# Performance work log

Hardware: AMD Instinct MI355X
Metric: run time of the kernel (lower is better)

Reference implementation:

```python
import jax, jax.numpy as jnp
import numpy as np
import math

B, S, D = 4, 2048, 1024
WINDOW = 10  # window_size; attends to |i-j| <= WINDOW//2


def setup_inputs() -> dict:
    key = jax.random.key(0)
    ks = jax.random.split(key, 9)
    sc = 1.0 / math.sqrt(D)
    return {
        "x": jax.random.normal(ks[0], (B, S, D), dtype=jnp.float32),
        "Wq": jax.random.normal(ks[1], (D, D), dtype=jnp.float32) * sc,
        "bq": jnp.zeros((D,), dtype=jnp.float32),
        "Wk": jax.random.normal(ks[2], (D, D), dtype=jnp.float32) * sc,
        "bk": jnp.zeros((D,), dtype=jnp.float32),
        "Wv": jax.random.normal(ks[3], (D, D), dtype=jnp.float32) * sc,
        "bv": jnp.zeros((D,), dtype=jnp.float32),
        "Wo": jax.random.normal(ks[4], (D, D), dtype=jnp.float32) * sc,
        "bo": jnp.zeros((D,), dtype=jnp.float32),
    }


def _local_mask(seq_len: int, window_size: int) -> jnp.ndarray:
    # row i attends to columns [i - w//2, i + w//2] inclusive -> |i - j| <= w//2
    i = jnp.arange(seq_len)[:, None]
    j = jnp.arange(seq_len)[None, :]
    return jnp.abs(i - j) <= (window_size // 2)  # [S, S] bool


def reference(x, Wq, bq, Wk, bk, Wv, bv, Wo, bo):
    # nn.Linear: y = x @ W.T + b
    Q = x @ Wq.T + bq  # [B, S, D]
    K = x @ Wk.T + bk
    V = x @ Wv.T + bv
    scores = jnp.einsum("bqd,bkd->bqk", Q, K) / jnp.float32(math.sqrt(D))
    mask = _local_mask(x.shape[1], WINDOW)
    scores = jnp.where(mask[None, :, :], scores, jnp.float32(-1e9))
    attn = jax.nn.softmax(scores, axis=-1)  # [B, S, S]
    context = jnp.einsum("bqk,bkd->bqd", attn, V)
    output = context @ Wo.T + bo
    return output, attn
```

## Files before the change

### kernel.cpp

```cpp
#include <hip/hip_runtime.h>
#include <hip/hip_bf16.h>
#include <cstdint>
#include <cstddef>


typedef __attribute__((ext_vector_type(8))) short bf16x8;
typedef __attribute__((ext_vector_type(4))) float f32x4;
typedef __attribute__((ext_vector_type(8))) unsigned short ushortx8;

#define GPTR(x) ((const __attribute__((address_space(1))) void*)(x))
#define LPTR(x) ((__attribute__((address_space(3))) void*)(x))

__device__ __forceinline__ unsigned short f2bf(float f) {
    __hip_bfloat16 h = __float2bfloat16(f);
    unsigned short u;
    __builtin_memcpy(&u, &h, 2);
    return u;
}
__device__ __forceinline__ float bf2f(unsigned short u) {
    unsigned int x = ((unsigned int)u) << 16;
    float f;
    __builtin_memcpy(&f, &x, 4);
    return f;
}

__global__ void prep1(const float* __restrict__ x,  const float* __restrict__ Wq,
                      const float* __restrict__ Wk, const float* __restrict__ Wv,
                      const float* __restrict__ Wo, const float* __restrict__ bv,
                      unsigned short* __restrict__ xh,
                      unsigned short* __restrict__ Woh,
                      unsigned short* __restrict__ Wqt,
                      unsigned short* __restrict__ Wkt,
                      unsigned short* __restrict__ Wvt,
                      float* __restrict__ bvo) {
    __shared__ float tl[64][65];
    const int bid = blockIdx.x;
    if (bid < 9216) {
        const int idx = bid * 256 + threadIdx.x;
        const float* src;
        unsigned short* dst;
        int off;
        if (idx < 2097152) { src = x;  dst = xh;  off = idx; }
        else               { src = Wo; dst = Woh; off = idx - 2097152; }
        f32x4 v = reinterpret_cast<const f32x4*>(src)[off];
        ushort4 o;
        o.x = f2bf(v[0]); o.y = f2bf(v[1]); o.z = f2bf(v[2]); o.w = f2bf(v[3]);
        reinterpret_cast<ushort4*>(dst)[off] = o;
    } else if (bid < 9984) {
        const int u   = bid - 9216;
        const int z   = u >> 8;
        const int rem = u & 255;
        const int by  = rem >> 4;
        const int bx  = rem & 15;
        const float* in = (z == 0) ? Wq : (z == 1) ? Wk : Wv;
        unsigned short* out = (z == 0) ? Wqt : (z == 1) ? Wkt : Wvt;
        const int t  = threadIdx.x;
        const int c  = t & 63;
        const int r4 = t >> 6;
#pragma unroll
        for (int i = 0; i < 16; ++i) {
            const int r = r4 * 16 + i;
            tl[r][c] = in[(size_t)(by * 64 + r) * 1024 + bx * 64 + c];
        }
        __syncthreads();
#pragma unroll
        for (int i = 0; i < 16; ++i) {
            const int r = r4 * 16 + i;
            out[(size_t)(bx * 64 + r) * 1024 + by * 64 + c] = f2bf(tl[c][r]);
        }
    } else {
        const int row  = (bid - 9984) * 4 + (threadIdx.x >> 6);
        const int lane = threadIdx.x & 63;
        float s = 0.f;
#pragma unroll
        for (int k = lane; k < 1024; k += 64)
            s += Wo[(size_t)row * 1024 + k] * bv[k];
#pragma unroll
        for (int off = 32; off >= 1; off >>= 1) s += __shfl_xor(s, off, 64);
        if (lane == 0) bvo[row] = s;
    }
}

__device__ __forceinline__ void gemm_core(const unsigned short* __restrict__ A,
                                          const unsigned short* __restrict__ Bw,
                                          int Kstride, int nk, int tm, int tn,
                                          unsigned short* As, unsigned short* Bs,
                                          f32x4 (&acc)[4][4]) {
    const int tid  = threadIdx.x;
    const int lane = tid & 63;
    const int w    = tid >> 6;
    const int wr   = w >> 1;
    const int wc   = w & 1;

    const int lrow8 = lane >> 3;
    const int lcolb = (lane & 7) << 4;

    const char* Abase = (const char*)(A + (size_t)tm * 128 * (size_t)Kstride);
    const char* Bbase = (const char*)(Bw + (size_t)tn * 128 * (size_t)Kstride);
    const size_t rstride = (size_t)Kstride * 2;

    for (int t = 0; t < nk; ++t) {
        const size_t k0b = ((size_t)t << 6) * 2;
#pragma unroll
        for (int ii = 0; ii < 4; ++ii) {
            const int c    = (w << 2) + ii;
            const int row  = (c << 3) + lrow8;
            const int csrc = lcolb ^ ((row & 7) << 4);
            __builtin_amdgcn_global_load_lds(
                GPTR(Abase + (size_t)row * rstride + k0b + (size_t)csrc),
                LPTR((char*)As + (c << 10)), 16, 0, 0);
            __builtin_amdgcn_global_load_lds(
                GPTR(Bbase + (size_t)row * rstride + k0b + (size_t)csrc),
                LPTR((char*)Bs + (c << 10)), 16, 0, 0);
        }
        __syncthreads();

#pragma unroll
        for (int kk = 0; kk < 2; ++kk) {
            bf16x8 af[4], bfr[4];
            const int cb = (kk << 6) + ((lane >> 4) << 4);
#pragma unroll
            for (int m = 0; m < 4; ++m) {
                const int row = (wr << 6) + (m << 4) + (lane & 15);
                af[m] = *reinterpret_cast<const bf16x8*>(
                    (const char*)As + row * 128 + (cb ^ ((row & 7) << 4)));
            }
#pragma unroll
            for (int n = 0; n < 4; ++n) {
                const int row = (wc << 6) + (n << 4) + (lane & 15);
                bfr[n] = *reinterpret_cast<const bf16x8*>(
                    (const char*)Bs + row * 128 + (cb ^ ((row & 7) << 4)));
            }
#pragma unroll
            for (int m = 0; m < 4; ++m)
#pragma unroll
                for (int n = 0; n < 4; ++n)
                    acc[m][n] = __builtin_amdgcn_mfma_f32_16x16x32_bf16(
                        af[m], bfr[n], acc[m][n], 0, 0, 0);
        }
        __syncthreads();
    }
}

__launch_bounds__(256, 3)
__global__ void splitk(const unsigned short* __restrict__ Wqt,
                       const unsigned short* __restrict__ Wkt,
                       const unsigned short* __restrict__ Woh,
                       const unsigned short* __restrict__ Wvt,
                       float* __restrict__ part) {
    __shared__ unsigned short As[128 * 64];
    __shared__ unsigned short Bs[128 * 64];
    f32x4 acc[4][4];
#pragma unroll
    for (int m = 0; m < 4; ++m)
#pragma unroll
        for (int n = 0; n < 4; ++n) acc[m][n] = (f32x4){0.f, 0.f, 0.f, 0.f};

    const int bid = blockIdx.x;
    const int mat = bid >> 8;
    const int loc = bid & 255;
    const int ks  = loc >> 6;
    const int t64 = loc & 63;
    const int tm  = t64 >> 3;
    const int tn  = t64 & 7;

    const unsigned short* A = mat ? Woh : Wqt;
    const unsigned short* B = mat ? Wvt : Wkt;
    gemm_core(A + ks * 256, B + ks * 256, 1024, 4, tm, tn, As, Bs, acc);

    float* dst = part + ((size_t)(mat * 4 + ks) << 20);
    const int lane = threadIdx.x & 63;
    const int w    = threadIdx.x >> 6;
    const int wr   = w >> 1, wc = w & 1;
    const int col0 = (tn << 7) + (wc << 6) + (lane & 15);
    const int row0 = (tm << 7) + (wr << 6) + ((lane >> 4) << 2);
#pragma unroll
    for (int n = 0; n < 4; ++n) {
        const int col = col0 + (n << 4);
#pragma unroll
        for (int m = 0; m < 4; ++m) {
            const int row = row0 + (m << 4);
#pragma unroll
            for (int r = 0; r < 4; ++r)
                dst[(size_t)(row + r) * 1024 + col] = acc[m][n][r];
        }
    }
}

__launch_bounds__(256, 4)
__global__ void redgemv(const float* __restrict__ part,
                        unsigned short* __restrict__ W2,
                        const unsigned short* __restrict__ Wqt,
                        const unsigned short* __restrict__ Wkt,
                        const float* __restrict__ bq, const float* __restrict__ bk,
                        float* __restrict__ w1, float* __restrict__ w2,
                        float* __restrict__ cbuf) {
    const int bid = blockIdx.x;
    if (bid < 2048) {
        const int u = bid * 256 + threadIdx.x;
        const int mat = u >> 18;
        const int off = u & 262143;
        const f32x4* p = reinterpret_cast<const f32x4*>(part);
        f32x4 s = p[((size_t)(mat * 4 + 0) << 18) + off];
        s += p[((size_t)(mat * 4 + 1) << 18) + off];
        s += p[((size_t)(mat * 4 + 2) << 18) + off];
        s += p[((size_t)(mat * 4 + 3) << 18) + off];
        ushort4 o;
        o.x = f2bf(s[0]); o.y = f2bf(s[1]); o.z = f2bf(s[2]); o.w = f2bf(s[3]);
        reinterpret_cast<ushort4*>(W2)[u] = o;
        return;
    }
    if (bid == 2304) {
        __shared__ float red[256];
        float pc = 0.f;
        for (int n = threadIdx.x; n < 1024; n += 256) pc += bq[n] * bk[n];
        red[threadIdx.x] = pc;
        __syncthreads();
        for (int s = 128; s > 0; s >>= 1) {
            if (threadIdx.x < s) red[threadIdx.x] += red[threadIdx.x + s];
            __syncthreads();
        }
        if (threadIdx.x == 0) cbuf[0] = red[0];
        return;
    }
    const int w    = threadIdx.x >> 6;
    const int lane = threadIdx.x & 63;
    const int d    = (bid - 2048) * 4 + w;
    const int n0   = lane << 4;
    const unsigned short* krow = Wkt + (size_t)d * 1024 + n0;
    const unsigned short* qrow = Wqt + (size_t)d * 1024 + n0;
    ushortx8 ka = *reinterpret_cast<const ushortx8*>(krow);
    ushortx8 kb = *reinterpret_cast<const ushortx8*>(krow + 8);
    ushortx8 qa = *reinterpret_cast<const ushortx8*>(qrow);
    ushortx8 qb = *reinterpret_cast<const ushortx8*>(qrow + 8);
    float a1 = 0.f, a2 = 0.f;
#pragma unroll
    for (int t = 0; t < 8; ++t) {
        a1 += bq[n0 + t] * bf2f(ka[t]) + bq[n0 + 8 + t] * bf2f(kb[t]);
        a2 += bk[n0 + t] * bf2f(qa[t]) + bk[n0 + 8 + t] * bf2f(qb[t]);
    }
#pragma unroll
    for (int off = 32; off >= 1; off >>= 1) {
        a1 += __shfl_xor(a1, off, 64);
        a2 += __shfl_xor(a2, off, 64);
    }
    if (lane == 0) { w1[d] = a1; w2[d] = a2; }
}

__launch_bounds__(256, 4)
__global__ void yv_r12(const unsigned short* __restrict__ A,
                       const unsigned short* __restrict__ Bw,
                       const float* __restrict__ bvo,
                       unsigned short* __restrict__ C,
                       const unsigned short* __restrict__ xh,
                       const float* __restrict__ w1, const float* __restrict__ w2,
                       const float* __restrict__ cbuf,
                       float* __restrict__ r1, float* __restrict__ r2) {
    __shared__ unsigned short As[128 * 64];
    __shared__ unsigned short Bs[128 * 64];
    const int bid = blockIdx.x;
    if (bid >= 1024) {
        const int w    = threadIdx.x >> 6;
        const int lane = threadIdx.x & 63;
        const int g    = (bid - 1024) * 4 + w;
        const unsigned short* row = xh + (size_t)g * 1024 + (lane << 4);
        ushortx8 xa = *reinterpret_cast<const ushortx8*>(row);
        ushortx8 xb = *reinterpret_cast<const ushortx8*>(row + 8);
        float a1 = 0.f, a2 = 0.f;
#pragma unroll
        for (int t = 0; t < 8; ++t) {
            const float xv = bf2f(xa[t]);
            const float xw = bf2f(xb[t]);
            a1 += xv * w1[(lane << 4) + t] + xw * w1[(lane << 4) + 8 + t];
            a2 += xv * w2[(lane << 4) + t] + xw * w2[(lane << 4) + 8 + t];
        }
#pragma unroll
        for (int off = 32; off >= 1; off >>= 1) {
            a1 += __shfl_xor(a1, off, 64);
            a2 += __shfl_xor(a2, off, 64);
        }
        if (lane == 0) { r1[g] = a1 + cbuf[0]; r2[g] = a2; }
        return;
    }

    f32x4 acc[4][4];
#pragma unroll
    for (int m = 0; m < 4; ++m)
#pragma unroll
        for (int n = 0; n < 4; ++n) acc[m][n] = (f32x4){0.f, 0.f, 0.f, 0.f};

    const int sid = (bid & 7) * 128 + (bid >> 3);
    const int tm  = sid >> 4;
    const int tn  = sid & 15;

    gemm_core(A, Bw, 1024, 16, tm, tn, As, Bs, acc);

    const int lane = threadIdx.x & 63;
    const int w    = threadIdx.x >> 6;
    const int wr   = w >> 1, wc = w & 1;
    const int seg  = tn >> 3;
    const int col0 = (tn << 7) + (wc << 6) + (lane & 15);
    const int row0 = (tm << 7) + (wr << 6) + ((lane >> 4) << 2);
#pragma unroll
    for (int n = 0; n < 4; ++n) {
        const int col = col0 + (n << 4);
        const float bb = seg ? bvo[col & 1023] : 0.f;
#pragma unroll
        for (int m = 0; m < 4; ++m) {
            const int row = row0 + (m << 4);
#pragma unroll
            for (int r = 0; r < 4; ++r)
                C[(size_t)(row + r) * 2048 + col] = f2bf(acc[m][n][r] + bb);
        }
    }
}

__launch_bounds__(256, 4)
__global__ void attn_band_kernel(const unsigned short* __restrict__ xh,
                                 const unsigned short* __restrict__ yVp,
                                 const float* __restrict__ r1,
                                 const float* __restrict__ r2,
                                 const float* __restrict__ bo,
                                 float* __restrict__ attn,
                                 float* __restrict__ outp) {
    __shared__ float psm[4][16];
    const int bid  = blockIdx.x;
    const int rb   = (bid & 7) * 256 + (bid >> 3);
    const int w    = threadIdx.x >> 6;
    const int lane = threadIdx.x & 63;
    const int g    = (rb << 2) + w;
    const int b    = g >> 11;
    const int i    = g & 2047;

    const unsigned short* qrow = xh + (size_t)g * 1024;
    float qf[16];
    {
        ushortx8 qa = *reinterpret_cast<const ushortx8*>(qrow + (lane << 4));
        ushortx8 qb = *reinterpret_cast<const ushortx8*>(qrow + (lane << 4) + 8);
#pragma unroll
        for (int t = 0; t < 8; ++t) { qf[t] = bf2f(qa[t]); qf[8 + t] = bf2f(qb[t]); }
    }
    const float r2g = r2[g];

    float s[11];
#pragma unroll
    for (int jj = 0; jj < 11; ++jj) {
        const int j = i - 5 + jj;
        const bool valid = ((unsigned)j < 2048u);
        const int jc = min(max(j, 0), 2047);
        const int gj = (b << 11) + jc;
        const unsigned short* krow = yVp + (size_t)gj * 2048;
        ushortx8 ka = *reinterpret_cast<const ushortx8*>(krow + (lane << 4));
        ushortx8 kb = *reinterpret_cast<const ushortx8*>(krow + (lane << 4) + 8);
        float d = 0.f;
#pragma unroll
        for (int t = 0; t < 8; ++t)
            d += qf[t] * bf2f(ka[t]) + qf[8 + t] * bf2f(kb[t]);
#pragma unroll
        for (int off = 32; off >= 1; off >>= 1) d += __shfl_xor(d, off, 64);
        s[jj] = valid ? (d + r2g + r1[gj]) * 0.03125f : -1e30f;
    }

    float mx = s[0];
#pragma unroll
    for (int jj = 1; jj < 11; ++jj) mx = fmaxf(mx, s[jj]);
    float p[11], sum = 0.f;
#pragma unroll
    for (int jj = 0; jj < 11; ++jj) { p[jj] = expf(s[jj] - mx); sum += p[jj]; }
    const float inv = 1.0f / sum;

    if (lane == 0) {
#pragma unroll
        for (int jj = 0; jj < 11; ++jj) psm[w][jj] = p[jj] * inv;
    }
    __syncthreads();

    const int lo = i - 5;
    float* arow = attn + (size_t)g * 2048;
#pragma unroll
    for (int e = 0; e < 8; ++e) {
        const int c0 = (e << 8) + (lane << 2);
        f32x4 v = (f32x4){0.f, 0.f, 0.f, 0.f};
        if (c0 + 3 >= lo && c0 <= lo + 10) {
#pragma unroll
            for (int t = 0; t < 4; ++t) {
                const int d = c0 + t - lo;
                if ((unsigned)d < 11u) v[t] = psm[w][d];
            }
        }
        *reinterpret_cast<f32x4*>(arow + c0) = v;
    }

    float cacc[16];
#pragma unroll
    for (int t = 0; t < 16; ++t) cacc[t] = 0.f;
#pragma unroll
    for (int jj = 0; jj < 11; ++jj) {
        const int j  = i - 5 + jj;
        const int jc = min(max(j, 0), 2047);
        const float pj = p[jj] * inv;
        const unsigned short* vrow = yVp + ((size_t)((b << 11) + jc)) * 2048 + 1024;
        ushortx8 va = *reinterpret_cast<const ushortx8*>(vrow + (lane << 4));
        ushortx8 vb = *reinterpret_cast<const ushortx8*>(vrow + (lane << 4) + 8);
#pragma unroll
        for (int t = 0; t < 8; ++t) {
            cacc[t]     += pj * bf2f(va[t]);
            cacc[8 + t] += pj * bf2f(vb[t]);
        }
    }
    const int c0 = lane << 4;
    float* op = outp + (size_t)g * 1024 + c0;
#pragma unroll
    for (int q = 0; q < 4; ++q) {
        f32x4 bb = *reinterpret_cast<const f32x4*>(bo + c0 + (q << 2));
        f32x4 o;
#pragma unroll
        for (int t = 0; t < 4; ++t) o[t] = cacc[(q << 2) + t] + bb[t];
        *reinterpret_cast<f32x4*>(op + (q << 2)) = o;
    }
}

extern "C" void kernel_launch(void* const* d_in, const int* in_sizes, int n_in,
                              void* d_out, int out_size, void* d_ws, size_t ws_size,
                              hipStream_t stream) {
    const float* x  = (const float*)d_in[0];
    const float* Wq = (const float*)d_in[1];
    const float* bq = (const float*)d_in[2];
    const float* Wk = (const float*)d_in[3];
    const float* bk = (const float*)d_in[4];
    const float* Wv = (const float*)d_in[5];
    const float* bv = (const float*)d_in[6];
    const float* Wo = (const float*)d_in[7];
    const float* bo = (const float*)d_in[8];

    const size_t MS = 8192, DD = 1024;

    float* out  = (float*)d_out;
    float* attn = out + MS * DD;

    char* ws = (char*)d_ws;
    unsigned short* xh   = (unsigned short*)ws; ws += MS * DD * 2;
    unsigned short* Woh  = (unsigned short*)ws; ws += DD * DD * 2;
    unsigned short* Wqt  = (unsigned short*)ws; ws += DD * DD * 2;
    unsigned short* Wkt  = (unsigned short*)ws; ws += DD * DD * 2;
    unsigned short* Wvt  = (unsigned short*)ws; ws += DD * DD * 2;
    float*          bvo  = (float*)ws;          ws += DD * 4;
    float*          w1   = (float*)ws;          ws += DD * 4;
    float*          w2   = (float*)ws;          ws += DD * 4;
    float*          cbuf = (float*)ws;          ws += 256;
    float*          r1   = (float*)ws;          ws += MS * 4;
    float*          r2   = (float*)ws;          ws += MS * 4;
    float*          part = (float*)ws;          ws += (size_t)8 * DD * DD * 4;
    unsigned short* W2   = (unsigned short*)ws; ws += 2 * DD * DD * 2;
    unsigned short* yVp  = (unsigned short*)ws; ws += MS * 2 * DD * 2;

    prep1<<<dim3(10240), dim3(256), 0, stream>>>(x, Wq, Wk, Wv, Wo, bv,
                                                 xh, Woh, Wqt, Wkt, Wvt, bvo);

    splitk<<<dim3(512), dim3(256), 0, stream>>>(Wqt, Wkt, Woh, Wvt, part);

    redgemv<<<dim3(2305), dim3(256), 0, stream>>>(part, W2, Wqt, Wkt, bq, bk,
                                                  w1, w2, cbuf);

    yv_r12<<<dim3(3072), dim3(256), 0, stream>>>(xh, W2, bvo, yVp,
                                                 xh, w1, w2, cbuf, r1, r2);

    attn_band_kernel<<<dim3(2048), dim3(256), 0, stream>>>(xh, yVp, r1, r2, bo,
                                                           attn, out);
}
```

Measured before the change: 119.1 us.

## Overlap x conversion and bias GEMVs with split-K weight GEMM blocks

```diff
diff --git a/kernel.cpp b/kernel.cpp
--- a/kernel.cpp
+++ b/kernel.cpp
@@ -24,32 +24,17 @@
     return f;
 }
 
-__global__ void prep1(const float* __restrict__ x,  const float* __restrict__ Wq,
-                      const float* __restrict__ Wk, const float* __restrict__ Wv,
-                      const float* __restrict__ Wo, const float* __restrict__ bv,
-                      unsigned short* __restrict__ xh,
-                      unsigned short* __restrict__ Woh,
+__global__ void prepW(const float* __restrict__ Wq, const float* __restrict__ Wk,
+                      const float* __restrict__ Wv, const float* __restrict__ Wo,
                       unsigned short* __restrict__ Wqt,
                       unsigned short* __restrict__ Wkt,
                       unsigned short* __restrict__ Wvt,
-                      float* __restrict__ bvo) {
+                      unsigned short* __restrict__ Woh) {
     __shared__ float tl[64][65];
     const int bid = blockIdx.x;
-    if (bid < 9216) {
-        const int idx = bid * 256 + threadIdx.x;
-        const float* src;
-        unsigned short* dst;
-        int off;
-        if (idx < 2097152) { src = x;  dst = xh;  off = idx; }
-        else               { src = Wo; dst = Woh; off = idx - 2097152; }
-        f32x4 v = reinterpret_cast<const f32x4*>(src)[off];
-        ushort4 o;
-        o.x = f2bf(v[0]); o.y = f2bf(v[1]); o.z = f2bf(v[2]); o.w = f2bf(v[3]);
-        reinterpret_cast<ushort4*>(dst)[off] = o;
-    } else if (bid < 9984) {
-        const int u   = bid - 9216;
-        const int z   = u >> 8;
-        const int rem = u & 255;
+    if (bid < 768) {
+        const int z   = bid >> 8;
+        const int rem = bid & 255;
         const int by  = rem >> 4;
         const int bx  = rem & 15;
         const float* in = (z == 0) ? Wq : (z == 1) ? Wk : Wv;
@@ -69,15 +54,11 @@
             out[(size_t)(bx * 64 + r) * 1024 + by * 64 + c] = f2bf(tl[c][r]);
         }
     } else {
-        const int row  = (bid - 9984) * 4 + (threadIdx.x >> 6);
-        const int lane = threadIdx.x & 63;
-        float s = 0.f;
-#pragma unroll
-        for (int k = lane; k < 1024; k += 64)
-            s += Wo[(size_t)row * 1024 + k] * bv[k];
-#pragma unroll
-        for (int off = 32; off >= 1; off >>= 1) s += __shfl_xor(s, off, 64);
-        if (lane == 0) bvo[row] = s;
+        const int off = (bid - 768) * 256 + threadIdx.x;
+        f32x4 v = reinterpret_cast<const f32x4*>(Wo)[off];
+        ushort4 o;
+        o.x = f2bf(v[0]); o.y = f2bf(v[1]); o.z = f2bf(v[2]); o.w = f2bf(v[3]);
+        reinterpret_cast<ushort4*>(Woh)[off] = o;
     }
 }
 
@@ -143,20 +124,81 @@
 }
 
 __launch_bounds__(256, 3)
-__global__ void splitk(const unsigned short* __restrict__ Wqt,
-                       const unsigned short* __restrict__ Wkt,
-                       const unsigned short* __restrict__ Woh,
-                       const unsigned short* __restrict__ Wvt,
-                       float* __restrict__ part) {
+__global__ void skx(const unsigned short* __restrict__ Wqt,
+                    const unsigned short* __restrict__ Wkt,
+                    const unsigned short* __restrict__ Woh,
+                    const unsigned short* __restrict__ Wvt,
+                    float* __restrict__ part,
+                    const float* __restrict__ x, unsigned short* __restrict__ xh,
+                    const float* __restrict__ Wo, const float* __restrict__ bv,
+                    float* __restrict__ bvo,
+                    const float* __restrict__ bq, const float* __restrict__ bk,
+                    float* __restrict__ w1, float* __restrict__ w2,
+                    float* __restrict__ cbuf) {
     __shared__ unsigned short As[128 * 64];
     __shared__ unsigned short Bs[128 * 64];
+    const int bid = blockIdx.x;
+    if (bid >= 512) {
+        if (bid < 8704) {
+            const int off = (bid - 512) * 256 + threadIdx.x;
+            f32x4 v = reinterpret_cast<const f32x4*>(x)[off];
+            ushort4 o;
+            o.x = f2bf(v[0]); o.y = f2bf(v[1]); o.z = f2bf(v[2]); o.w = f2bf(v[3]);
+            reinterpret_cast<ushort4*>(xh)[off] = o;
+        } else if (bid < 8960) {
+            const int row  = (bid - 8704) * 4 + (threadIdx.x >> 6);
+            const int lane = threadIdx.x & 63;
+            float s = 0.f;
+#pragma unroll
+            for (int k = lane; k < 1024; k += 64)
+                s += Wo[(size_t)row * 1024 + k] * bv[k];
+#pragma unroll
+            for (int off = 32; off >= 1; off >>= 1) s += __shfl_xor(s, off, 64);
+            if (lane == 0) bvo[row] = s;
+        } else if (bid < 9216) {
+            const int w    = threadIdx.x >> 6;
+            const int lane = threadIdx.x & 63;
+            const int d    = (bid - 8960) * 4 + w;
+            const int n0   = lane << 4;
+            const unsigned short* krow = Wkt + (size_t)d * 1024 + n0;
+            const unsigned short* qrow = Wqt + (size_t)d * 1024 + n0;
+            ushortx8 ka = *reinterpret_cast<const ushortx8*>(krow);
+            ushortx8 kb = *reinterpret_cast<const ushortx8*>(krow + 8);
+            ushortx8 qa = *reinterpret_cast<const ushortx8*>(qrow);
+            ushortx8 qb = *reinterpret_cast<const ushortx8*>(qrow + 8);
+            float a1 = 0.f, a2 = 0.f;
+#pragma unroll
+            for (int t = 0; t < 8; ++t) {
+                a1 += bq[n0 + t] * bf2f(ka[t]) + bq[n0 + 8 + t] * bf2f(kb[t]);
+                a2 += bk[n0 + t] * bf2f(qa[t]) + bk[n0 + 8 + t] * bf2f(qb[t]);
+            }
+#pragma unroll
+            for (int off = 32; off >= 1; off >>= 1) {
+                a1 += __shfl_xor(a1, off, 64);
+                a2 += __shfl_xor(a2, off, 64);
+            }
+            if (lane == 0) { w1[d] = a1; w2[d] = a2; }
+        } else {
+            __shared__ float red[256];
+            float pc = 0.f;
+            for (int n = threadIdx.x; n < 1024; n += 256) pc += bq[n] * bk[n];
+            red[threadIdx.x] = pc;
+            __syncthreads();
+            for (int s = 128; s > 0; s >>= 1) {
+                if (threadIdx.x < s) red[threadIdx.x] += red[threadIdx.x + s];
+                __syncthreads();
+            }
+            if (threadIdx.x == 0) cbuf[0] = red[0];
+        }
+        return;
+    }
+
     f32x4 acc[4][4];
 #pragma unroll
     for (int m = 0; m < 4; ++m)
 #pragma unroll
         for (int n = 0; n < 4; ++n) acc[m][n] = (f32x4){0.f, 0.f, 0.f, 0.f};
 
-    const int bid = blockIdx.x;
     const int mat = bid >> 8;
     const int loc = bid & 255;
     const int ks  = loc >> 6;
@@ -187,64 +229,19 @@
     }
 }
 
-__launch_bounds__(256, 4)
-__global__ void redgemv(const float* __restrict__ part,
-                        unsigned short* __restrict__ W2,
-                        const unsigned short* __restrict__ Wqt,
-                        const unsigned short* __restrict__ Wkt,
-                        const float* __restrict__ bq, const float* __restrict__ bk,
-                        float* __restrict__ w1, float* __restrict__ w2,
-                        float* __restrict__ cbuf) {
-    const int bid = blockIdx.x;
-    if (bid < 2048) {
-        const int u = bid * 256 + threadIdx.x;
-        const int mat = u >> 18;
-        const int off = u & 262143;
-        const f32x4* p = reinterpret_cast<const f32x4*>(part);
-        f32x4 s = p[((size_t)(mat * 4 + 0) << 18) + off];
-        s += p[((size_t)(mat * 4 + 1) << 18) + off];
-        s += p[((size_t)(mat * 4 + 2) << 18) + off];
-        s += p[((size_t)(mat * 4 + 3) << 18) + off];
-        ushort4 o;
-        o.x = f2bf(s[0]); o.y = f2bf(s[1]); o.z = f2bf(s[2]); o.w = f2bf(s[3]);
-        reinterpret_cast<ushort4*>(W2)[u] = o;
-        return;
-    }
-    if (bid == 2304) {
-        __shared__ float red[256];
-        float pc = 0.f;
-        for (int n = threadIdx.x; n < 1024; n += 256) pc += bq[n] * bk[n];
-        red[threadIdx.x] = pc;
-        __syncthreads();
-        for (int s = 128; s > 0; s >>= 1) {
-            if (threadIdx.x < s) red[threadIdx.x] += red[threadIdx.x + s];
-            __syncthreads();
-        }
-        if (threadIdx.x == 0) cbuf[0] = red[0];
-        return;
-    }
-    const int w    = threadIdx.x >> 6;
-    const int lane = threadIdx.x & 63;
-    const int d    = (bid - 2048) * 4 + w;
-    const int n0   = lane << 4;
-    const unsigned short* krow = Wkt + (size_t)d * 1024 + n0;
-    const unsigned short* qrow = Wqt + (size_t)d * 1024 + n0;
-    ushortx8 ka = *reinterpret_cast<const ushortx8*>(krow);
-    ushortx8 kb = *reinterpret_cast<const ushortx8*>(krow + 8);
-    ushortx8 qa = *reinterpret_cast<const ushortx8*>(qrow);
-    ushortx8 qb = *reinterpret_cast<const ushortx8*>(qrow + 8);
-    float a1 = 0.f, a2 = 0.f;
-#pragma unroll
-    for (int t = 0; t < 8; ++t) {
-        a1 += bq[n0 + t] * bf2f(ka[t]) + bq[n0 + 8 + t] * bf2f(kb[t]);
-        a2 += bk[n0 + t] * bf2f(qa[t]) + bk[n0 + 8 + t] * bf2f(qb[t]);
-    }
-#pragma unroll
-    for (int off = 32; off >= 1; off >>= 1) {
-        a1 += __shfl_xor(a1, off, 64);
-        a2 += __shfl_xor(a2, off, 64);
-    }
-    if (lane == 0) { w1[d] = a1; w2[d] = a2; }
+__global__ void reduce_wp(const float* __restrict__ part,
+                          unsigned short* __restrict__ W2) {
+    const int u = blockIdx.x * 256 + threadIdx.x;
+    const int mat = u >> 18;
+    const int off = u & 262143;
+    const f32x4* p = reinterpret_cast<const f32x4*>(part);
+    f32x4 s = p[((size_t)(mat * 4 + 0) << 18) + off];
+    s += p[((size_t)(mat * 4 + 1) << 18) + off];
+    s += p[((size_t)(mat * 4 + 2) << 18) + off];
+    s += p[((size_t)(mat * 4 + 3) << 18) + off];
+    ushort4 o;
+    o.x = f2bf(s[0]); o.y = f2bf(s[1]); o.z = f2bf(s[2]); o.w = f2bf(s[3]);
+    reinterpret_cast<ushort4*>(W2)[u] = o;
 }
 
 __launch_bounds__(256, 4)
@@ -454,13 +451,14 @@
     unsigned short* W2   = (unsigned short*)ws; ws += 2 * DD * DD * 2;
     unsigned short* yVp  = (unsigned short*)ws; ws += MS * 2 * DD * 2;
 
-    prep1<<<dim3(10240), dim3(256), 0, stream>>>(x, Wq, Wk, Wv, Wo, bv,
-                                                 xh, Woh, Wqt, Wkt, Wvt, bvo);
-
-    splitk<<<dim3(512), dim3(256), 0, stream>>>(Wqt, Wkt, Woh, Wvt, part);
-
-    redgemv<<<dim3(2305), dim3(256), 0, stream>>>(part, W2, Wqt, Wkt, bq, bk,
-                                                  w1, w2, cbuf);
+    prepW<<<dim3(1792), dim3(256), 0, stream>>>(Wq, Wk, Wv, Wo,
+                                                Wqt, Wkt, Wvt, Woh);
+
+    skx<<<dim3(9217), dim3(256), 0, stream>>>(Wqt, Wkt, Woh, Wvt, part,
+                                              x, xh, Wo, bv, bvo,
+                                              bq, bk, w1, w2, cbuf);
+
+    reduce_wp<<<dim3(2048), dim3(256), 0, stream>>>(part, W2);
 
     yv_r12<<<dim3(3072), dim3(256), 0, stream>>>(xh, W2, bvo, yVp,
                                                  xh, w1, w2, cbuf, r1, r2);
```

Result: no change. 117.0 us (-1.7%).
